# Optimization experiments

Hardware: AMD Instinct MI355X
Metric: run time of the kernel (lower is better)

Reference implementation:

```python
import jax, jax.numpy as jnp
import numpy as np

EPS = 1e-6
NUM_HEADS = 16


def _layer_norm(x):
    # LayerNorm32: fp32 layernorm, eps=1e-6, no affine params
    m = jnp.mean(x, axis=-1, keepdims=True)
    v = jnp.var(x, axis=-1, keepdims=True)
    return (x - m) * jax.lax.rsqrt(v + EPS)


def setup_inputs() -> dict:
    key = jax.random.key(0)
    ks = jax.random.split(key, 6)
    B, L, C = 4, 2048, 1024
    H = 4 * C
    s = 0.02
    return {
        "x": jax.random.normal(ks[0], (B, L, C), dtype=jnp.float32),
        "qkv_w": jax.random.normal(ks[1], (C, 3 * C), dtype=jnp.float32) * s,
        "qkv_b": jnp.zeros((3 * C,), dtype=jnp.float32),
        "proj_w": jax.random.normal(ks[2], (C, C), dtype=jnp.float32) * s,
        "proj_b": jnp.zeros((C,), dtype=jnp.float32),
        "fc1_w": jax.random.normal(ks[3], (C, H), dtype=jnp.float32) * s,
        "fc1_b": jnp.zeros((H,), dtype=jnp.float32),
        "fc2_w": jax.random.normal(ks[4], (H, C), dtype=jnp.float32) * s,
        "fc2_b": jnp.zeros((C,), dtype=jnp.float32),
    }


def _block(x, qkv_w, qkv_b, proj_w, proj_b, fc1_w, fc1_b, fc2_w, fc2_b):
    B, L, C = x.shape
    Hn = NUM_HEADS
    D = C // Hn

    # --- attention branch (pre-norm) ---
    h = _layer_norm(x)
    qkv = h @ qkv_w + qkv_b                      # [B, L, 3C]
    qkv = qkv.reshape(B, L, 3, Hn, D)
    q, k, v = qkv[:, :, 0], qkv[:, :, 1], qkv[:, :, 2]  # [B, L, Hn, D]
    scale = 1.0 / jnp.sqrt(jnp.asarray(D, dtype=x.dtype))
    logits = jnp.einsum("bqhd,bkhd->bhqk", q, k) * scale
    attn = jax.nn.softmax(logits, axis=-1)
    o = jnp.einsum("bhqk,bkhd->bqhd", attn, v).reshape(B, L, C)
    o = o @ proj_w + proj_b
    x = x + o

    # --- MLP branch (pre-norm) ---
    h = _layer_norm(x)
    h = jax.nn.gelu(h @ fc1_w + fc1_b, approximate=True)  # tanh GELU
    h = h @ fc2_w + fc2_b
    return x + h


def reference(x, qkv_w, qkv_b, proj_w, proj_b, fc1_w, fc1_b, fc2_w, fc2_b):
    return _block(x, qkv_w, qkv_b, proj_w, proj_b, fc1_w, fc1_b, fc2_w, fc2_b)
```

## Files before the change

kernel.cpp:

```cpp
#include <hip/hip_runtime.h>
#include <hip/hip_bf16.h>

typedef float f32x4 __attribute__((ext_vector_type(4)));
typedef __bf16 bf16x8 __attribute__((ext_vector_type(8)));
typedef unsigned short us8 __attribute__((ext_vector_type(8)));

#define MBYTE (1ull << 20)

#define QSCALE_LOG2E 0.18033688011112042f
#define GELU_K 2.3022081902f

__device__ __forceinline__ unsigned short f2bf(float f) {
    __bf16 h = (__bf16)f;
    return __builtin_bit_cast(unsigned short, h);
}

__device__ __forceinline__ float fast_exp2(float x) {
    return __builtin_amdgcn_exp2f(x);
}

__device__ __forceinline__ f32x4 mfma16(bf16x8 a, bf16x8 b, f32x4 c) {
    return __builtin_amdgcn_mfma_f32_16x16x32_bf16(a, b, c, 0, 0, 0);
}

__device__ __forceinline__ void gload16(const void* g, void* l) {
    __builtin_amdgcn_global_load_lds(
        (const __attribute__((address_space(1))) unsigned int*)g,
        (__attribute__((address_space(3))) unsigned int*)l, 16, 0, 0);
}

__global__ __launch_bounds__(256) void ln_kernel(const float* __restrict__ x,
                                                 unsigned short* __restrict__ out) {
    int row = blockIdx.x;
    int t = threadIdx.x;
    const float* xr = x + (size_t)row * 1024;
    float4 v = *(const float4*)(xr + t * 4);
    float s = v.x + v.y + v.z + v.w;
    float ss = v.x * v.x + v.y * v.y + v.z * v.z + v.w * v.w;
    #pragma unroll
    for (int off = 1; off < 64; off <<= 1) {
        s += __shfl_xor(s, off);
        ss += __shfl_xor(ss, off);
    }
    __shared__ float ps[4], pss[4];
    int wid = t >> 6, lane = t & 63;
    if (lane == 0) { ps[wid] = s; pss[wid] = ss; }
    __syncthreads();
    s = ps[0] + ps[1] + ps[2] + ps[3];
    ss = pss[0] + pss[1] + pss[2] + pss[3];
    float mean = s * (1.0f / 1024.0f);
    float var = ss * (1.0f / 1024.0f) - mean * mean;
    float rs = rsqrtf(var + 1e-6f);
    ushort4 ov;
    ov.x = f2bf((v.x - mean) * rs);
    ov.y = f2bf((v.y - mean) * rs);
    ov.z = f2bf((v.z - mean) * rs);
    ov.w = f2bf((v.w - mean) * rs);
    *(ushort4*)(out + (size_t)row * 1024 + t * 4) = ov;
}

__global__ __launch_bounds__(256) void convT_kernel(const float* __restrict__ W,
                                                    unsigned short* __restrict__ Wt,
                                                    int K, int N) {
    __shared__ float tile[32][33];
    int t = threadIdx.x;
    int tx = t & 31, ty = t >> 5;
    int bx = blockIdx.x, by = blockIdx.y;
    #pragma unroll
    for (int r = 0; r < 4; r++) {
        int row = by * 32 + ty + r * 8;
        int col = bx * 32 + tx;
        tile[ty + r * 8][tx] = W[(size_t)row * N + col];
    }
    __syncthreads();
    #pragma unroll
    for (int r = 0; r < 4; r++) {
        int orow = bx * 32 + ty + r * 8;
        int ocol = by * 32 + tx;
        Wt[(size_t)orow * K + ocol] = f2bf(tile[tx][ty + r * 8]);
    }
}

__global__ __launch_bounds__(256) void vT_kernel(const unsigned short* __restrict__ qkv,
                                                 unsigned short* __restrict__ vT) {
    __shared__ unsigned short tile[32][34];
    int t = threadIdx.x;
    int tx = t & 31, ty = t >> 5;
    int lt = blockIdx.x, dt = blockIdx.y, bh = blockIdx.z;
    int b = bh >> 4, h = bh & 15;
    const unsigned short* src = qkv + (size_t)(b * 2048 + lt * 32) * 3072 + 2048 + h * 64 + dt * 32;
    #pragma unroll
    for (int r = 0; r < 4; r++)
        tile[ty + r * 8][tx] = src[(size_t)(ty + r * 8) * 3072 + tx];
    __syncthreads();
    int perm = (lt & 1) * 32 + ((tx >> 2) & 3) * 8 + ((tx >> 4) & 1) * 4 + (tx & 3);
    unsigned short* dst = vT + ((size_t)bh * 64 + dt * 32) * 2048 + (size_t)(lt >> 1) * 64;
    #pragma unroll
    for (int r = 0; r < 4; r++)
        dst[(size_t)(ty + r * 8) * 2048 + perm] = tile[tx][ty + r * 8];
}

template <int EPI>
__global__ __launch_bounds__(256) void gemm_bt(const unsigned short* __restrict__ A,
                                               const unsigned short* __restrict__ Bt,
                                               const float* __restrict__ bias,
                                               const float* __restrict__ res,
                                               float* __restrict__ outF,
                                               unsigned short* __restrict__ outB,
                                               int M, int N, int K) {
    __shared__ __align__(16) unsigned short As[2][128 * 32];
    __shared__ __align__(16) unsigned short Bs[2][128 * 32];
    int t = threadIdx.x;
    int lane = t & 63, wid = t >> 6;

    int gx = gridDim.x;
    int nwg = gx * gridDim.y;
    int orig = blockIdx.y * gx + blockIdx.x;
    int cpx = nwg >> 3;
    int swz = (orig & 7) * cpx + (orig >> 3);
    int bm = swz / gx, bn = swz % gx;

    int wm = wid >> 1, wn = wid & 1;
    f32x4 acc[4][4] = {};

    int sub = lane >> 2;
    int schunk = ((lane & 3) ^ ((lane >> 3) & 3)) * 8;
    const unsigned short* gA0 = A + (size_t)(bm * 128 + wid * 32 + sub) * K + schunk;
    const unsigned short* gA1 = gA0 + (size_t)16 * K;
    const unsigned short* gB0 = Bt + (size_t)(bn * 128 + wid * 32 + sub) * K + schunk;
    const unsigned short* gB1 = gB0 + (size_t)16 * K;

    int ql = lane & 15;
    int rchunk = (((lane >> 4) ^ ((lane >> 1) & 3))) * 8;

    const int NT = K >> 5;
    gload16(gA0, &As[0][(wid * 32) * 32]);
    gload16(gA1, &As[0][(wid * 32 + 16) * 32]);
    gload16(gB0, &Bs[0][(wid * 32) * 32]);
    gload16(gB1, &Bs[0][(wid * 32 + 16) * 32]);
    __syncthreads();

    int cur = 0;
    for (int tt = 0; tt < NT; ++tt) {
        if (tt + 1 < NT) {
            int k0 = (tt + 1) << 5;
            int nb = cur ^ 1;
            gload16(gA0 + k0, &As[nb][(wid * 32) * 32]);
            gload16(gA1 + k0, &As[nb][(wid * 32 + 16) * 32]);
            gload16(gB0 + k0, &Bs[nb][(wid * 32) * 32]);
            gload16(gB1 + k0, &Bs[nb][(wid * 32 + 16) * 32]);
        }
        bf16x8 af[4], bfr[4];
        #pragma unroll
        for (int m = 0; m < 4; m++)
            af[m] = *(const bf16x8*)&As[cur][(wm * 64 + m * 16 + ql) * 32 + rchunk];
        #pragma unroll
        for (int n = 0; n < 4; n++)
            bfr[n] = *(const bf16x8*)&Bs[cur][(wn * 64 + n * 16 + ql) * 32 + rchunk];
        __builtin_amdgcn_s_setprio(1);
        #pragma unroll
        for (int m = 0; m < 4; m++)
            #pragma unroll
            for (int n = 0; n < 4; n++)
                acc[m][n] = mfma16(af[m], bfr[n], acc[m][n]);
        __builtin_amdgcn_s_setprio(0);
        __syncthreads();
        cur ^= 1;
    }

    #pragma unroll
    for (int m = 0; m < 4; m++) {
        #pragma unroll
        for (int n = 0; n < 4; n++) {
            int col = bn * 128 + wn * 64 + n * 16 + ql;
            float bv = bias[col];
            #pragma unroll
            for (int r = 0; r < 4; r++) {
                int row = bm * 128 + wm * 64 + m * 16 + (lane >> 4) * 4 + r;
                float val = acc[m][n][r] + bv;
                if (EPI == 0) {
                    if (col < 1024) val *= QSCALE_LOG2E;
                    outB[(size_t)row * N + col] = f2bf(val);
                } else if (EPI == 1) {
                    float w = val + 0.044715f * val * val * val;
                    float g = val / (1.0f + fast_exp2(-GELU_K * w));
                    outB[(size_t)row * N + col] = f2bf(g);
                } else {
                    outF[(size_t)row * N + col] = val + res[(size_t)row * N + col];
                }
            }
        }
    }
}

__global__ __launch_bounds__(256) void attn_kernel(const unsigned short* __restrict__ qkv,
                                                   const unsigned short* __restrict__ vT,
                                                   unsigned short* __restrict__ o) {
    int bid = blockIdx.x;
    int qb = bid & 31;
    int bh = bid >> 5;
    int b = bh >> 4, h = bh & 15;
    int t = threadIdx.x, lane = t & 63, wid = t >> 6;

    const unsigned short* base = qkv + (size_t)b * 2048 * 3072 + h * 64;
    const unsigned short* vbase = vT + (size_t)bh * 64 * 2048;

    __shared__ __align__(16) unsigned short Ks[2][2][64][32];
    __shared__ __align__(16) unsigned short Vs[2][2][64][32];

    int ql = lane & 15;
    int hi = lane >> 4;

    bf16x8 qf[2];
    {
        int qrow = qb * 64 + wid * 16 + ql;
        const unsigned short* qp = base + (size_t)qrow * 3072 + hi * 8;
        qf[0] = *(const bf16x8*)(qp);
        qf[1] = *(const bf16x8*)(qp + 32);
    }

    us8 ones_u;
    #pragma unroll
    for (int j = 0; j < 8; j++) ones_u[j] = 0x3F80;
    bf16x8 ones = __builtin_bit_cast(bf16x8, ones_u);

    f32x4 accO[4] = {};
    f32x4 lacc = {};

    int srow = wid * 16 + (lane >> 2);
    int schunk = ((lane & 3) ^ ((lane >> 3) & 3)) * 8;
    const unsigned short* gk = base + 1024 + (size_t)srow * 3072 + schunk;
    const unsigned short* gv = vbase + (size_t)srow * 2048 + schunk;

    auto STAGE = [&](int buf, int kt) {
        const unsigned short* pk = gk + (size_t)kt * 64 * 3072;
        const unsigned short* pv = gv + (size_t)kt * 64;
        gload16(pk, &Ks[buf][0][wid * 16][0]);
        gload16(pk + 32, &Ks[buf][1][wid * 16][0]);
        gload16(pv, &Vs[buf][0][wid * 16][0]);
        gload16(pv + 32, &Vs[buf][1][wid * 16][0]);
    };

    int rchunk = (hi ^ ((ql >> 1) & 3)) * 8;

    STAGE(0, 0);
    asm volatile("s_waitcnt vmcnt(0)" ::: "memory");
    __builtin_amdgcn_sched_barrier(0);
    __builtin_amdgcn_s_barrier();

    int buf = 0;
    for (int kt = 0; kt < 32; kt++) {
        if (kt + 1 < 32) STAGE(buf ^ 1, kt + 1);

        f32x4 s0 = {}, s1 = {}, s2 = {}, s3 = {};
        #pragma unroll
        for (int c = 0; c < 2; c++) {
            bf16x8 a0 = *(const bf16x8*)&Ks[buf][c][ 0 + ql][rchunk];
            bf16x8 a1 = *(const bf16x8*)&Ks[buf][c][16 + ql][rchunk];
            bf16x8 a2 = *(const bf16x8*)&Ks[buf][c][32 + ql][rchunk];
            bf16x8 a3 = *(const bf16x8*)&Ks[buf][c][48 + ql][rchunk];
            s0 = mfma16(a0, qf[c], s0);
            s1 = mfma16(a1, qf[c], s1);
            s2 = mfma16(a2, qf[c], s2);
            s3 = mfma16(a3, qf[c], s3);
        }

        us8 pu0, pu1;
        #pragma unroll
        for (int j = 0; j < 4; j++) {
            pu0[j]     = f2bf(fast_exp2(s0[j]));
            pu0[4 + j] = f2bf(fast_exp2(s1[j]));
            pu1[j]     = f2bf(fast_exp2(s2[j]));
            pu1[4 + j] = f2bf(fast_exp2(s3[j]));
        }
        bf16x8 paf0 = __builtin_bit_cast(bf16x8, pu0);
        bf16x8 paf1 = __builtin_bit_cast(bf16x8, pu1);

        #pragma unroll
        for (int nn = 0; nn < 4; nn++) {
            bf16x8 bv0 = *(const bf16x8*)&Vs[buf][0][nn * 16 + ql][rchunk];
            bf16x8 bv1 = *(const bf16x8*)&Vs[buf][1][nn * 16 + ql][rchunk];
            accO[nn] = mfma16(paf0, bv0, accO[nn]);
            accO[nn] = mfma16(paf1, bv1, accO[nn]);
        }
        lacc = mfma16(paf0, ones, lacc);
        lacc = mfma16(paf1, ones, lacc);

        asm volatile("s_waitcnt vmcnt(0)" ::: "memory");
        __builtin_amdgcn_sched_barrier(0);
        __builtin_amdgcn_s_barrier();
        buf ^= 1;
    }

    #pragma unroll
    for (int r = 0; r < 4; r++) {
        float rq = 1.0f / lacc[r];
        int row = qb * 64 + wid * 16 + hi * 4 + r;
        #pragma unroll
        for (int nn = 0; nn < 4; nn++) {
            int col = h * 64 + nn * 16 + ql;
            o[(size_t)(b * 2048 + row) * 1024 + col] = f2bf(accO[nn][r] * rq);
        }
    }
}

extern "C" void kernel_launch(void* const* d_in, const int* in_sizes, int n_in,
                              void* d_out, int out_size, void* d_ws, size_t ws_size,
                              hipStream_t stream) {
    const float* x      = (const float*)d_in[0];
    const float* qkv_w  = (const float*)d_in[1];
    const float* qkv_b  = (const float*)d_in[2];
    const float* proj_w = (const float*)d_in[3];
    const float* proj_b = (const float*)d_in[4];
    const float* fc1_w  = (const float*)d_in[5];
    const float* fc1_b  = (const float*)d_in[6];
    const float* fc2_w  = (const float*)d_in[7];
    const float* fc2_b  = (const float*)d_in[8];
    float* out = (float*)d_out;

    char* ws = (char*)d_ws;
    unsigned short* h_buf   = (unsigned short*)(ws + 0 * MBYTE);
    unsigned short* qkv_buf = (unsigned short*)(ws + 16 * MBYTE);
    unsigned short* o_buf   = (unsigned short*)(ws + 64 * MBYTE);
    float*          x2_buf  = (float*)(ws + 80 * MBYTE);
    unsigned short* vT_buf  = (unsigned short*)(ws + 80 * MBYTE);
    unsigned short* wqT     = (unsigned short*)(ws + 112 * MBYTE);
    unsigned short* wpT     = (unsigned short*)(ws + 118 * MBYTE);
    unsigned short* w1T     = (unsigned short*)(ws + 120 * MBYTE);
    unsigned short* w2T     = (unsigned short*)(ws + 128 * MBYTE);
    unsigned short* g_buf   = (unsigned short*)(ws + 16 * MBYTE);

    const int M = 8192;

    convT_kernel<<<dim3(3072 / 32, 1024 / 32), 256, 0, stream>>>(qkv_w, wqT, 1024, 3072);
    convT_kernel<<<dim3(1024 / 32, 1024 / 32), 256, 0, stream>>>(proj_w, wpT, 1024, 1024);
    convT_kernel<<<dim3(4096 / 32, 1024 / 32), 256, 0, stream>>>(fc1_w, w1T, 1024, 4096);
    convT_kernel<<<dim3(1024 / 32, 4096 / 32), 256, 0, stream>>>(fc2_w, w2T, 4096, 1024);

    ln_kernel<<<M, 256, 0, stream>>>(x, h_buf);

    gemm_bt<0><<<dim3(3072 / 128, M / 128), 256, 0, stream>>>(
        h_buf, wqT, qkv_b, nullptr, nullptr, qkv_buf, M, 3072, 1024);

    vT_kernel<<<dim3(64, 2, 64), 256, 0, stream>>>(qkv_buf, vT_buf);

    attn_kernel<<<dim3(32 * 64), 256, 0, stream>>>(qkv_buf, vT_buf, o_buf);

    gemm_bt<2><<<dim3(1024 / 128, M / 128), 256, 0, stream>>>(
        o_buf, wpT, proj_b, x, x2_buf, nullptr, M, 1024, 1024);

    ln_kernel<<<M, 256, 0, stream>>>(x2_buf, h_buf);

    gemm_bt<1><<<dim3(4096 / 128, M / 128), 256, 0, stream>>>(
        h_buf, w1T, fc1_b, nullptr, nullptr, g_buf, M, 4096, 1024);

    gemm_bt<2><<<dim3(1024 / 128, M / 128), 256, 0, stream>>>(
        g_buf, w2T, fc2_b, x2_buf, out, nullptr, M, 1024, 4096);
}
```

Baseline: 438.3 us.

## Load GEMM B fragments directly from global into registers, bypassing LDS

The GEMM now stages only the A tile through LDS, while each wave loads its B operand fragments straight from global memory into registers, double-buffered across k-steps. Explicit vmcnt waits and raw s_barrier replace __syncthreads so the register prefetch overlaps the MFMA work. This halves LDS traffic and LDS footprint, which may raise occupancy. In exchange, B rows are read redundantly by the two waves sharing wn, with less coalesced 16-byte loads, and the hand-written waitcnt counts assume a particular load ordering.

```diff
diff --git a/kernel.cpp b/kernel.cpp
--- a/kernel.cpp
+++ b/kernel.cpp
@@ -109,7 +109,6 @@
                                                unsigned short* __restrict__ outB,
                                                int M, int N, int K) {
     __shared__ __align__(16) unsigned short As[2][128 * 32];
-    __shared__ __align__(16) unsigned short Bs[2][128 * 32];
     int t = threadIdx.x;
     int lane = t & 63, wid = t >> 6;
 
@@ -121,51 +120,64 @@
     int bm = swz / gx, bn = swz % gx;
 
     int wm = wid >> 1, wn = wid & 1;
+    int ql = lane & 15, hi = lane >> 4;
     f32x4 acc[4][4] = {};
 
     int sub = lane >> 2;
     int schunk = ((lane & 3) ^ ((lane >> 3) & 3)) * 8;
     const unsigned short* gA0 = A + (size_t)(bm * 128 + wid * 32 + sub) * K + schunk;
     const unsigned short* gA1 = gA0 + (size_t)16 * K;
-    const unsigned short* gB0 = Bt + (size_t)(bn * 128 + wid * 32 + sub) * K + schunk;
-    const unsigned short* gB1 = gB0 + (size_t)16 * K;
-
-    int ql = lane & 15;
-    int rchunk = (((lane >> 4) ^ ((lane >> 1) & 3))) * 8;
+    unsigned short* lA0[2] = { &As[0][(wid * 32) * 32], &As[1][(wid * 32) * 32] };
+    unsigned short* lA1[2] = { &As[0][(wid * 32 + 16) * 32], &As[1][(wid * 32 + 16) * 32] };
+
+    int rchunk = (hi ^ ((ql >> 1) & 3)) * 8;
+
+    const unsigned short* gBf = Bt + (size_t)(bn * 128 + wn * 64 + ql) * K + hi * 8;
 
     const int NT = K >> 5;
-    gload16(gA0, &As[0][(wid * 32) * 32]);
-    gload16(gA1, &As[0][(wid * 32 + 16) * 32]);
-    gload16(gB0, &Bs[0][(wid * 32) * 32]);
-    gload16(gB1, &Bs[0][(wid * 32 + 16) * 32]);
-    __syncthreads();
-
-    int cur = 0;
-    for (int tt = 0; tt < NT; ++tt) {
-        if (tt + 1 < NT) {
-            int k0 = (tt + 1) << 5;
-            int nb = cur ^ 1;
-            gload16(gA0 + k0, &As[nb][(wid * 32) * 32]);
-            gload16(gA1 + k0, &As[nb][(wid * 32 + 16) * 32]);
-            gload16(gB0 + k0, &Bs[nb][(wid * 32) * 32]);
-            gload16(gB1 + k0, &Bs[nb][(wid * 32 + 16) * 32]);
-        }
-        bf16x8 af[4], bfr[4];
+
+    bf16x8 bA[4], bB[4];
+
+    gload16(gA0, lA0[0]);
+    gload16(gA1, lA1[0]);
+    #pragma unroll
+    for (int n = 0; n < 4; n++)
+        bA[n] = *(const bf16x8*)(gBf + (size_t)n * 16 * K);
+    asm volatile("s_waitcnt vmcnt(0)" ::: "memory");
+    __builtin_amdgcn_sched_barrier(0);
+    __builtin_amdgcn_s_barrier();
+
+    auto kstep = [&](int cur, int tt, bf16x8 (&bc)[4], bf16x8 (&bn_)[4]) {
+        bool st = (tt + 1 < NT);
+        if (st) {
+            int k0n = (tt + 1) << 5;
+            gload16(gA0 + k0n, lA0[cur ^ 1]);
+            gload16(gA1 + k0n, lA1[cur ^ 1]);
+            __builtin_amdgcn_sched_barrier(0);
+            #pragma unroll
+            for (int n = 0; n < 4; n++)
+                bn_[n] = *(const bf16x8*)(gBf + (size_t)n * 16 * K + k0n);
+        }
+        bf16x8 af[4];
         #pragma unroll
         for (int m = 0; m < 4; m++)
             af[m] = *(const bf16x8*)&As[cur][(wm * 64 + m * 16 + ql) * 32 + rchunk];
-        #pragma unroll
-        for (int n = 0; n < 4; n++)
-            bfr[n] = *(const bf16x8*)&Bs[cur][(wn * 64 + n * 16 + ql) * 32 + rchunk];
         __builtin_amdgcn_s_setprio(1);
         #pragma unroll
         for (int m = 0; m < 4; m++)
             #pragma unroll
             for (int n = 0; n < 4; n++)
-                acc[m][n] = mfma16(af[m], bfr[n], acc[m][n]);
+                acc[m][n] = mfma16(af[m], bc[n], acc[m][n]);
         __builtin_amdgcn_s_setprio(0);
-        __syncthreads();
-        cur ^= 1;
+        if (st) asm volatile("s_waitcnt vmcnt(4)" ::: "memory");
+        else    asm volatile("s_waitcnt vmcnt(0)" ::: "memory");
+        __builtin_amdgcn_sched_barrier(0);
+        __builtin_amdgcn_s_barrier();
+    };
+
+    for (int tt = 0; tt < NT; tt += 2) {
+        kstep(0, tt, bA, bB);
+        kstep(1, tt + 1, bB, bA);
     }
 
     #pragma unroll
@@ -176,7 +188,7 @@
             float bv = bias[col];
             #pragma unroll
             for (int r = 0; r < 4; r++) {
-                int row = bm * 128 + wm * 64 + m * 16 + (lane >> 4) * 4 + r;
+                int row = bm * 128 + wm * 64 + m * 16 + hi * 4 + r;
                 float val = acc[m][n][r] + bv;
                 if (EPI == 0) {
                     if (col < 1024) val *= QSCALE_LOG2E;
```

Result: slower. 590.2 us (+34.7%).
